# Kernel optimization log

Hardware: AMD Instinct MI355X
Metric: run time of the kernel (lower is better)

Reference implementation:

```python
import jax, jax.numpy as jnp
import numpy as np


def sparsemax_last(z):
    """Sparsemax over the last axis (Martins & Astudillo 2016)."""
    dims = z.shape[-1]
    z_sorted = jnp.sort(z, axis=-1)[..., ::-1]          # descending
    z_cumsum = jnp.cumsum(z_sorted, axis=-1)
    k = jnp.arange(1, dims + 1, dtype=z.dtype)
    support = 1.0 + k * z_sorted > z_cumsum              # [..., dims] bool
    k_z = jnp.sum(support.astype(jnp.int32), axis=-1)    # support size >= 1 for finite z
    tau_sum = jnp.take_along_axis(z_cumsum, (k_z - 1)[..., None], axis=-1)[..., 0]
    tau = (tau_sum - 1.0) / k_z.astype(z.dtype)
    return jnp.maximum(z - tau[..., None], 0.0)


def _bin_codes_1hot(depth, dtype):
    n_leaf = 2 ** depth
    indices = np.arange(n_leaf)
    offsets = 2 ** np.arange(depth)
    codes = (indices[None, :] // offsets[:, None]) % 2   # [depth, 2^depth]
    onehot = np.stack([codes, 1 - codes], axis=-1)       # [depth, 2^depth, 2]
    return jnp.asarray(onehot, dtype=dtype)


def setup_inputs() -> dict:
    key = jax.random.key(0)
    ks = jax.random.split(key, 5)
    B, I, N, D, U = 1024, 256, 512, 6, 16
    return {
        "x": jax.random.normal(ks[0], (B, I), dtype=jnp.float32),
        "feature_selection_logits": jax.random.normal(ks[1], (I, N, D), dtype=jnp.float32),
        "feature_thresholds": jax.random.normal(ks[2], (N, D), dtype=jnp.float32),
        "log_temperatures": jax.random.normal(ks[3], (N, D), dtype=jnp.float32) * 0.1,
        "response": jax.random.normal(ks[4], (N, U, 2 ** D), dtype=jnp.float32),
    }


def reference(x, feature_selection_logits, feature_thresholds, log_temperatures, response):
    depth = feature_thresholds.shape[1]
    # feature selection via sparsemax over depth axis (axis=-1, as in source)
    feature_selectors = sparsemax_last(feature_selection_logits)          # [I,N,D]
    feature_values = jnp.einsum('bi,ind->bnd', x, feature_selectors)      # [B,N,D]
    # temperature-scaled threshold logits
    tl = (feature_values - feature_thresholds) * jnp.exp(-log_temperatures)
    tl = jnp.stack([-tl, tl], axis=-1)                                    # [B,N,D,2]
    bins = jnp.clip(0.5 * tl + 0.5, 0.0, 1.0)                             # sparsemoid
    onehot = _bin_codes_1hot(depth, bins.dtype)                           # [D,2^D,2]
    bin_matches = jnp.einsum('btds,dcs->btdc', bins, onehot)              # [B,N,D,2^D]
    response_weights = jnp.prod(bin_matches, axis=-2)                     # [B,N,2^D]
    out = jnp.einsum('bnd,ncd->bnc', response_weights, response)          # [B,N,U]
    return jnp.sum(out, axis=1)                                           # [B,U]
```

## Files before the change

### kernel.cpp

```cpp
#include <hip/hip_runtime.h>
#include <hip/hip_bf16.h>

#define B_SZ 1024
#define I_SZ 256
#define N_SZ 512
#define D_SZ 6
#define U_SZ 16
#define C_SZ 64
#define NSPLIT 64

typedef __bf16 bf16_t;
typedef bf16_t bf16x8 __attribute__((ext_vector_type(8)));
typedef float  f32x4  __attribute__((ext_vector_type(4)));


__global__ __launch_bounds__(256) void prep_pack(
    const float* __restrict__ fsl, const float* __restrict__ x,
    const float* __restrict__ resp,
    bf16_t* __restrict__ selF, bf16_t* __restrict__ xbF,
    bf16_t* __restrict__ respF) {
  __shared__ float smem[4160];
  const int bid = blockIdx.x, t = threadIdx.x;

  if (bid < 512) {
    float (*sT)[17] = (float(*)[17])smem;
    const int nb = bid & 31, ib = bid >> 5;
    const int i_loc = t >> 4, n_loc = t & 15;
    const int n0 = nb * 16, i0 = ib * 16;

    const float* z = fsl + ((size_t)(i0 + i_loc) * N_SZ + (n0 + n_loc)) * D_SZ;
    float v[D_SZ], s[D_SZ];
#pragma unroll
    for (int d = 0; d < D_SZ; ++d) { v[d] = z[d]; s[d] = v[d]; }
#define CSWAP(a, b) { float hi = fmaxf(s[a], s[b]); float lo = fminf(s[a], s[b]); s[a] = hi; s[b] = lo; }
#pragma unroll
    for (int r = 0; r < 3; ++r) {
      CSWAP(0, 1) CSWAP(2, 3) CSWAP(4, 5)
      CSWAP(1, 2) CSWAP(3, 4)
    }
#undef CSWAP
    float cs[D_SZ];
    cs[0] = s[0];
#pragma unroll
    for (int j = 1; j < D_SZ; ++j) cs[j] = cs[j - 1] + s[j];
    int kz = 0;
#pragma unroll
    for (int j = 0; j < D_SZ; ++j)
      kz += (1.0f + (float)(j + 1) * s[j] > cs[j]) ? 1 : 0;
    const float tau = (cs[kz - 1] - 1.0f) / (float)kz;
#pragma unroll
    for (int d = 0; d < D_SZ; ++d)
      sT[n_loc * 6 + d][i_loc] = fmaxf(v[d] - tau, 0.0f);
    __syncthreads();

    if (t < 192) {
      const int r = t >> 1, h = t & 1;
      const int g  = 6 * nb + (r >> 4), lm = r & 15;
      const int kk = ib >> 1, q = (ib & 1) * 2 + h;
      bf16x8 o;
#pragma unroll
      for (int jj = 0; jj < 8; ++jj) o[jj] = (bf16_t)sT[r][h * 8 + jj];
      *(bf16x8*)(selF + ((size_t)(g * 8 + kk) * 64 + q * 16 + lm) * 8) = o;
    }
  } else if (bid < 576) {
    float (*xs)[257] = (float(*)[257])smem;
    const int gb = bid - 512;
#pragma unroll
    for (int c = 0; c < 4; ++c) {
      const int e = c * 256 + t;
      const int row = e >> 6, col = (e & 63) * 4;
      const float4 v = *(const float4*)(x + (size_t)(gb * 16 + row) * I_SZ + col);
      xs[row][col] = v.x; xs[row][col + 1] = v.y;
      xs[row][col + 2] = v.z; xs[row][col + 3] = v.w;
    }
    __syncthreads();
#pragma unroll
    for (int h = 0; h < 2; ++h) {
      const int fid = h * 256 + t;
      const int kk = fid >> 6, lane = fid & 63;
      const int lm = lane & 15, q = lane >> 4;
      bf16x8 o;
#pragma unroll
      for (int jj = 0; jj < 8; ++jj) o[jj] = (bf16_t)xs[lm][kk * 32 + q * 8 + jj];
      *(bf16x8*)(xbF + ((size_t)(gb * 8 + kk) * 64 + lane) * 8) = o;
    }
  } else {
    float (*rs)[16][65] = (float(*)[16][65])smem;
    const int n0 = (bid - 576) * 4;
#pragma unroll
    for (int c = 0; c < 4; ++c) {
      const int e = c * 256 + t;
      const int n_loc = e >> 8, idx = (e & 255) * 4;
      const int u = idx >> 6, cc = idx & 63;
      const float4 v = *(const float4*)(resp + (size_t)(n0 + n_loc) * 1024 + idx);
      rs[n_loc][u][cc] = v.x; rs[n_loc][u][cc + 1] = v.y;
      rs[n_loc][u][cc + 2] = v.z; rs[n_loc][u][cc + 3] = v.w;
    }
    __syncthreads();
#pragma unroll
    for (int h = 0; h < 2; ++h) {
      const int fid = h * 256 + t;
      const int n_loc = fid >> 7, chunk = (fid >> 6) & 1, lane = fid & 63;
      const int lm = lane & 15, q = lane >> 4;
      bf16x8 o;
#pragma unroll
      for (int jj = 0; jj < 8; ++jj)
        o[jj] = (bf16_t)rs[n_loc][lm][chunk * 32 + q * 8 + jj];
      *(bf16x8*)(respF + ((size_t)((n0 + n_loc) * 2 + chunk) * 64 + lane) * 8) = o;
    }
  }
}

__global__ __launch_bounds__(256, 4) void fused_k(
    const bf16_t* __restrict__ selF,
    const bf16_t* __restrict__ xbF,
    const float* __restrict__ th,
    const float* __restrict__ lt,
    const bf16_t* __restrict__ respF,
    float* __restrict__ part) {
  __shared__ float fv[48][68];
  const int t = threadIdx.x;
  const int lane = t & 63, wave = t >> 6;
  const int lm = lane & 15, q = lane >> 4;
  const int btile = blockIdx.x & 15, ns = blockIdx.x >> 4;

  if (wave < 3) {
    f32x4 acc[4];
#pragma unroll
    for (int s = 0; s < 4; ++s) acc[s] = (f32x4){0.f, 0.f, 0.f, 0.f};
    const int g = ns * 3 + wave;
    const bf16_t* aF = selF + ((size_t)g * 8 * 64 + lane) * 8;
    const bf16_t* bF = xbF + ((size_t)btile * 4 * 8 * 64 + lane) * 8;
#pragma unroll
    for (int kk = 0; kk < 8; ++kk) {
      const bf16x8 a = *(const bf16x8*)(aF + (size_t)kk * 64 * 8);
#pragma unroll
      for (int s = 0; s < 4; ++s) {
        const bf16x8 bv = *(const bf16x8*)(bF + (size_t)(s * 8 + kk) * 64 * 8);
        acc[s] = __builtin_amdgcn_mfma_f32_16x16x32_bf16(a, bv, acc[s], 0, 0, 0);
      }
    }
    float thv[4], ev[4];
#pragma unroll
    for (int r = 0; r < 4; ++r) {
      const int kp = ns * 48 + wave * 16 + q * 4 + r;
      thv[r] = th[kp]; ev[r] = __expf(-lt[kp]);
    }
#pragma unroll
    for (int s = 0; s < 4; ++s)
#pragma unroll
      for (int r = 0; r < 4; ++r)
        fv[wave * 16 + q * 4 + r][s * 16 + lm] = (acc[s][r] - thv[r]) * ev[r];
  }
  __syncthreads();

  f32x4 acc = (f32x4){0.f, 0.f, 0.f, 0.f};
  const int bloc = wave * 16 + lm;

#pragma unroll
  for (int j = 0; j < 8; ++j) {
    const int n = ns * 8 + j;
    const bf16_t* rF = respF + ((size_t)n * 2 * 64 + lane) * 8;
    const bf16x8 bv0 = *(const bf16x8*)(rF);
    const bf16x8 bv1 = *(const bf16x8*)(rF + 64 * 8);

    float b0v[D_SZ], b1v[D_SZ];
#pragma unroll
    for (int d = 0; d < D_SZ; ++d) {
      const float tl = fv[j * 6 + d][bloc];
      b1v[d] = fminf(fmaxf(0.5f * tl + 0.5f, 0.0f), 1.0f);
      b0v[d] = fminf(fmaxf(0.5f - 0.5f * tl, 0.0f), 1.0f);
    }
    float p2[2], p4[4], p8[8];
    p2[0] = b1v[0]; p2[1] = b0v[0];
#pragma unroll
    for (int i = 0; i < 4; ++i) p4[i] = p2[i & 1] * ((i & 2) ? b0v[1] : b1v[1]);
#pragma unroll
    for (int i = 0; i < 8; ++i) p8[i] = p4[i & 3] * ((i & 4) ? b0v[2] : b1v[2]);
    const float f3 = (q & 1) ? b0v[3] : b1v[3];
    const float f4 = (q & 2) ? b0v[4] : b1v[4];
    const float fq = f3 * f4;
    const float g0 = fq * b1v[5];
    const float g1 = fq * b0v[5];

    bf16x8 a0, a1;
#pragma unroll
    for (int jj = 0; jj < 8; ++jj) {
      a0[jj] = (bf16_t)(p8[jj] * g0);
      a1[jj] = (bf16_t)(p8[jj] * g1);
    }
    acc = __builtin_amdgcn_mfma_f32_16x16x32_bf16(a0, bv0, acc, 0, 0, 0);
    acc = __builtin_amdgcn_mfma_f32_16x16x32_bf16(a1, bv1, acc, 0, 0, 0);
  }

#pragma unroll
  for (int r = 0; r < 4; ++r)
    part[(size_t)ns * (B_SZ * U_SZ) +
         (size_t)(btile * 64 + wave * 16 + q * 4 + r) * U_SZ + lm] = acc[r];
}

__global__ __launch_bounds__(256) void reduce_k(
    const float* __restrict__ part, float* __restrict__ out) {
  __shared__ float red[4][64];
  const int t = threadIdx.x;
  const int o = blockIdx.x * 64 + (t & 63);
  const int g = t >> 6;
  float s = 0.0f;
#pragma unroll
  for (int k = 0; k < 16; ++k)
    s += part[(size_t)(g * 16 + k) * (B_SZ * U_SZ) + o];
  red[g][t & 63] = s;
  __syncthreads();
  if (t < 64)
    out[blockIdx.x * 64 + t] = red[0][t] + red[1][t] + red[2][t] + red[3][t];
}

extern "C" void kernel_launch(void* const* d_in, const int* in_sizes, int n_in,
                              void* d_out, int out_size, void* d_ws, size_t ws_size,
                              hipStream_t stream) {
  const float* x    = (const float*)d_in[0];
  const float* fsl  = (const float*)d_in[1];
  const float* th   = (const float*)d_in[2];
  const float* lt   = (const float*)d_in[3];
  const float* resp = (const float*)d_in[4];
  float* out = (float*)d_out;

  char* w = (char*)d_ws;
  bf16_t* selF  = (bf16_t*)(w);
  bf16_t* xbF   = (bf16_t*)(w + 1572864);
  bf16_t* respF = (bf16_t*)(w + 2097152);
  float*  part  = (float*)(w + 3145728);

  prep_pack<<<704, 256, 0, stream>>>(fsl, x, resp, selF, xbF, respF);

  fused_k<<<16 * NSPLIT, 256, 0, stream>>>(selF, xbF, th, lt, respF, part);

  reduce_k<<<(B_SZ * U_SZ) / 64, 256, 0, stream>>>(part, out);
}
```

Baseline: 80.12 us.

## Replace partial-sum buffer and reduce kernel with atomic accumulation; rebalance GEMM over waves

Drops the separate reduce kernel and the 4 MB partial buffer. Each fused block now atomically adds its tile into the output, which extra blocks in the prep kernel zero first. The first-stage GEMM is also rebalanced so all four waves work: each wave handles one batch sub-tile across three feature groups, where before three waves each covered four batch sub-tiles. Atomic adds from 64 splits per output element may contend and make the float summation order nondeterministic.

```diff
diff --git a/kernel.cpp b/kernel.cpp
--- a/kernel.cpp
+++ b/kernel.cpp
@@ -18,7 +18,7 @@
     const float* __restrict__ fsl, const float* __restrict__ x,
     const float* __restrict__ resp,
     bf16_t* __restrict__ selF, bf16_t* __restrict__ xbF,
-    bf16_t* __restrict__ respF) {
+    bf16_t* __restrict__ respF, float* __restrict__ out) {
   __shared__ float smem[4160];
   const int bid = blockIdx.x, t = threadIdx.x;
 
@@ -84,7 +84,7 @@
       for (int jj = 0; jj < 8; ++jj) o[jj] = (bf16_t)xs[lm][kk * 32 + q * 8 + jj];
       *(bf16x8*)(xbF + ((size_t)(gb * 8 + kk) * 64 + lane) * 8) = o;
     }
-  } else {
+  } else if (bid < 704) {
     float (*rs)[16][65] = (float(*)[16][65])smem;
     const int n0 = (bid - 576) * 4;
 #pragma unroll
@@ -108,6 +108,9 @@
         o[jj] = (bf16_t)rs[n_loc][lm][chunk * 32 + q * 8 + jj];
       *(bf16x8*)(respF + ((size_t)((n0 + n_loc) * 2 + chunk) * 64 + lane) * 8) = o;
     }
+  } else {
+    const int idx = ((bid - 704) * 256 + t) * 4;
+    *(float4*)(out + idx) = make_float4(0.f, 0.f, 0.f, 0.f);
   }
 }
 
@@ -117,40 +120,40 @@
     const float* __restrict__ th,
     const float* __restrict__ lt,
     const bf16_t* __restrict__ respF,
-    float* __restrict__ part) {
+    float* __restrict__ out) {
   __shared__ float fv[48][68];
   const int t = threadIdx.x;
   const int lane = t & 63, wave = t >> 6;
   const int lm = lane & 15, q = lane >> 4;
   const int btile = blockIdx.x & 15, ns = blockIdx.x >> 4;
 
-  if (wave < 3) {
-    f32x4 acc[4];
-#pragma unroll
-    for (int s = 0; s < 4; ++s) acc[s] = (f32x4){0.f, 0.f, 0.f, 0.f};
-    const int g = ns * 3 + wave;
-    const bf16_t* aF = selF + ((size_t)g * 8 * 64 + lane) * 8;
-    const bf16_t* bF = xbF + ((size_t)btile * 4 * 8 * 64 + lane) * 8;
+  {
+    f32x4 acc[3];
+#pragma unroll
+    for (int kg = 0; kg < 3; ++kg) acc[kg] = (f32x4){0.f, 0.f, 0.f, 0.f};
+    const bf16_t* aF = selF + ((size_t)(ns * 3) * 8 * 64 + lane) * 8;
+    const bf16_t* bF = xbF + ((size_t)(btile * 4 + wave) * 8 * 64 + lane) * 8;
 #pragma unroll
     for (int kk = 0; kk < 8; ++kk) {
-      const bf16x8 a = *(const bf16x8*)(aF + (size_t)kk * 64 * 8);
-#pragma unroll
-      for (int s = 0; s < 4; ++s) {
-        const bf16x8 bv = *(const bf16x8*)(bF + (size_t)(s * 8 + kk) * 64 * 8);
-        acc[s] = __builtin_amdgcn_mfma_f32_16x16x32_bf16(a, bv, acc[s], 0, 0, 0);
+      const bf16x8 bv = *(const bf16x8*)(bF + (size_t)kk * 64 * 8);
+#pragma unroll
+      for (int kg = 0; kg < 3; ++kg) {
+        const bf16x8 a = *(const bf16x8*)(aF + (size_t)(kg * 8 + kk) * 64 * 8);
+        acc[kg] = __builtin_amdgcn_mfma_f32_16x16x32_bf16(a, bv, acc[kg], 0, 0, 0);
       }
     }
-    float thv[4], ev[4];
-#pragma unroll
-    for (int r = 0; r < 4; ++r) {
-      const int kp = ns * 48 + wave * 16 + q * 4 + r;
-      thv[r] = th[kp]; ev[r] = __expf(-lt[kp]);
-    }
-#pragma unroll
-    for (int s = 0; s < 4; ++s)
+#pragma unroll
+    for (int kg = 0; kg < 3; ++kg) {
+      float thv[4], ev[4];
+#pragma unroll
+      for (int r = 0; r < 4; ++r) {
+        const int kp = ns * 48 + kg * 16 + q * 4 + r;
+        thv[r] = th[kp]; ev[r] = __expf(-lt[kp]);
+      }
 #pragma unroll
       for (int r = 0; r < 4; ++r)
-        fv[wave * 16 + q * 4 + r][s * 16 + lm] = (acc[s][r] - thv[r]) * ev[r];
+        fv[kg * 16 + q * 4 + r][wave * 16 + lm] = (acc[kg][r] - thv[r]) * ev[r];
+    }
   }
   __syncthreads();
 
@@ -193,26 +196,10 @@
     acc = __builtin_amdgcn_mfma_f32_16x16x32_bf16(a1, bv1, acc, 0, 0, 0);
   }
 
+  float* obase = out + (size_t)(btile * 64 + wave * 16) * U_SZ;
 #pragma unroll
   for (int r = 0; r < 4; ++r)
-    part[(size_t)ns * (B_SZ * U_SZ) +
-         (size_t)(btile * 64 + wave * 16 + q * 4 + r) * U_SZ + lm] = acc[r];
-}
-
-__global__ __launch_bounds__(256) void reduce_k(
-    const float* __restrict__ part, float* __restrict__ out) {
-  __shared__ float red[4][64];
-  const int t = threadIdx.x;
-  const int o = blockIdx.x * 64 + (t & 63);
-  const int g = t >> 6;
-  float s = 0.0f;
-#pragma unroll
-  for (int k = 0; k < 16; ++k)
-    s += part[(size_t)(g * 16 + k) * (B_SZ * U_SZ) + o];
-  red[g][t & 63] = s;
-  __syncthreads();
-  if (t < 64)
-    out[blockIdx.x * 64 + t] = red[0][t] + red[1][t] + red[2][t] + red[3][t];
+    atomicAdd(&obase[(q * 4 + r) * U_SZ + lm], acc[r]);
 }
 
 extern "C" void kernel_launch(void* const* d_in, const int* in_sizes, int n_in,
@@ -229,11 +216,8 @@
   bf16_t* selF  = (bf16_t*)(w);
   bf16_t* xbF   = (bf16_t*)(w + 1572864);
   bf16_t* respF = (bf16_t*)(w + 2097152);
-  float*  part  = (float*)(w + 3145728);
-
-  prep_pack<<<704, 256, 0, stream>>>(fsl, x, resp, selF, xbF, respF);
-
-  fused_k<<<16 * NSPLIT, 256, 0, stream>>>(selF, xbF, th, lt, respF, part);
-
-  reduce_k<<<(B_SZ * U_SZ) / 64, 256, 0, stream>>>(part, out);
+
+  prep_pack<<<720, 256, 0, stream>>>(fsl, x, resp, selF, xbF, respF, out);
+
+  fused_k<<<16 * NSPLIT, 256, 0, stream>>>(selF, xbF, th, lt, respF, out);
 }
```

After: 77.83 us. 2.9% less time.
